# Kernel tuning notes

Hardware: AMD Instinct MI355X
Metric: run time of the kernel (lower is better)

The kernel has to match this reference:

```python
import jax, jax.numpy as jnp
import numpy as np

N_QUBITS = 12
LAYERS = 3


def _apply(state, mats, axes):
    """Apply batched k-qubit gate. state: [B]+[2]*n complex64; mats: [B, 2^k, 2^k]; axes: state axes (1-based)."""
    k = len(axes)
    d = 2 ** k
    s = jnp.moveaxis(state, axes, tuple(range(1, k + 1)))
    shp = s.shape
    s = jnp.einsum('bij,bjk->bik', mats, s.reshape(shp[0], d, -1))
    return jnp.moveaxis(s.reshape(shp), tuple(range(1, k + 1)), axes)


def _ry(theta):
    # RY(theta) = [[cos(t/2), -sin(t/2)], [sin(t/2), cos(t/2)]], batched over B
    c = jnp.cos(theta / 2).astype(jnp.complex64)
    s = jnp.sin(theta / 2).astype(jnp.complex64)
    return jnp.stack([jnp.stack([c, -s], -1), jnp.stack([s, c], -1)], -2)


def _crx(theta):
    # CRX: identity on control=0 subspace, RX(theta) on control=1 subspace (basis order |ct>)
    c = jnp.cos(theta / 2).astype(jnp.complex64)
    s = (-1j) * jnp.sin(theta / 2).astype(jnp.complex64)
    o = jnp.ones_like(c)
    z = jnp.zeros_like(c)
    rows = [[o, z, z, z], [z, o, z, z], [z, z, c, s], [z, z, s, c]]
    return jnp.stack([jnp.stack(r, -1) for r in rows], -2)


def _circuit(state_re, state_im, params):
    B = params.shape[0]
    n = N_QUBITS
    state = (state_re + 1j * state_im).astype(jnp.complex64).reshape((B,) + (2,) * n)
    p = params.reshape(B, LAYERS, 4, n)  # param idx order: RY block, CRX block, RY block, CRX block
    for l in range(LAYERS):
        th = p[:, l]
        for w in range(n):
            state = _apply(state, _ry(th[:, 0, w]), (w + 1,))
        for i, w in enumerate(reversed(range(n))):
            state = _apply(state, _crx(th[:, 1, i]), (w + 1, ((w + 1) % n) + 1))
        for w in range(n):
            state = _apply(state, _ry(th[:, 2, w]), (w + 1,))
        for i, w in enumerate([n - 1] + list(range(n - 1))):
            state = _apply(state, _crx(th[:, 3, i]), (w + 1, ((w - 1) % n) + 1))
    state = state.reshape(B, -1)
    return jnp.stack([state.real, state.imag], -1)  # [B, 2^n, 2]


def setup_inputs() -> dict:
    key = jax.random.key(0)
    k1, k2, k3 = jax.random.split(key, 3)
    B = 128
    dim = 2 ** N_QUBITS
    return {
        'state_re': jax.random.normal(k1, (B, dim), jnp.float32),
        'state_im': jax.random.normal(k2, (B, dim), jnp.float32),
        'params': jax.random.normal(k3, (B, LAYERS * 4 * N_QUBITS), jnp.float32),
    }


def reference(state_re, state_im, params):
    return _circuit(state_re, state_im, params)
```

## Files before the change

### kernel.cpp

```cpp
#include <hip/hip_runtime.h>
#include <math.h>

#define DIM  4096
#define BLK  512
#define NPAR 144

typedef float v2f __attribute__((ext_vector_type(2)));

struct Ph { int reg[3]; int wav[3]; };
struct TMap { unsigned pk[9]; unsigned short so[8]; unsigned short rn[8]; };

constexpr int REGS[12][3] = {
  {11,0,1},{1,2,3},{3,4,5},{5,6,7},{7,8,9},{9,10,11},
  {11,0,1},{9,10,11},{7,8,9},{5,6,7},{3,4,5},{1,2,3}};

constexpr Ph phaseAt(int i) {
  Ph p = {};
  if (i == 0 || i == 37) {
    p.reg[0]=0; p.reg[1]=1; p.reg[2]=2;
    p.wav[0]=9; p.wav[1]=10; p.wav[2]=11;
    return p;
  }
  int e = (i - 1) % 12;
  for (int j = 0; j < 3; ++j) p.reg[j] = REGS[e][j];
  bool A = (e <= 2) || (e >= 10);
  p.wav[0] = A ? 6 : 2; p.wav[1] = A ? 7 : 3; p.wav[2] = A ? 8 : 4;
  return p;
}
constexpr bool inArr(const int* a, int n, int b) {
  for (int i = 0; i < n; ++i) if (a[i] == b) return true;
  return false;
}
constexpr int idxOf3(const int* a, int v) {
  for (int j = 0; j < 3; ++j) if (a[j] == v) return j;
  return -1;
}
constexpr bool isLoc(int t) {
  if (t == 0 || t == 36) return false;
  Ph a = phaseAt(t), b = phaseAt(t + 1);
  return a.wav[0]==b.wav[0] && a.wav[1]==b.wav[1] && a.wav[2]==b.wav[2];
}
constexpr int bufIdx(int t) {
  int k = 0;
  for (int u = 0; u <= t; ++u) if (!isLoc(u)) ++k;
  return (k + 1) & 1;
}
constexpr int sharedBit(Ph o, Ph n) {
  for (int j = 0; j < 3; ++j) if (inArr(n.reg, 3, o.reg[j])) return o.reg[j];
  return -1;
}

struct BuildOut { TMap m; int js, jn; bool ok; };

constexpr BuildOut buildT(Ph o, Ph n, bool local) {
  BuildOut R = {};
  R.ok = true;
  int s = sharedBit(o, n);
  if (s < 0) { R.ok = false; return R; }
  R.js = idxOf3(o.reg, s);
  R.jn = idxOf3(n.reg, s);
  if (R.js < 0 || R.jn < 0) { R.ok = false; return R; }
  bool lo[12] = {}, ln[12] = {};
  for (int b = 0; b < 12; ++b) {
    lo[b] = !inArr(o.reg,3,b) && !inArr(o.wav,3,b);
    ln[b] = !inArr(n.reg,3,b) && !inArr(n.wav,3,b);
  }
  int col[12] = {};
  bool uo[12] = {}, un[12] = {}, consumed[12] = {};
  col[s] = 1; consumed[s] = true;
  int row = 1;
  for (int b = 0; b < 12 && row < 4; ++b)
    if (lo[b] && ln[b]) { col[b] = 1 << row; uo[b]=un[b]=true; consumed[b]=true; ++row; }
  while (row < 4) {
    int a = -1, c = -1;
    for (int b = 0; b < 12; ++b) if (lo[b] && !uo[b] && !consumed[b]) { a = b; break; }
    for (int b = 0; b < 12; ++b) if (ln[b] && !un[b] && !consumed[b] && b != a) { c = b; break; }
    if (a < 0 || c < 0) { R.ok = false; return R; }
    col[a] |= 1 << row; col[c] |= 1 << row;
    uo[a]=true; un[c]=true; consumed[c]=true;
    ++row;
  }
  if (local) {
    for (int i = 0; i < 3; ++i) {
      if (consumed[o.wav[i]]) { R.ok = false; return R; }
      col[o.wav[i]] |= 1 << (9 + i);
      consumed[o.wav[i]] = true;
    }
    int rr = 4;
    for (int b = 0; b < 12; ++b) if (!consumed[b]) { col[b] |= 1 << rr; ++rr; }
    if (rr != 9) { R.ok = false; return R; }
  } else {
    int rr = 4;
    for (int b = 0; b < 12; ++b) if (!consumed[b]) { col[b] |= 1 << rr; ++rr; }
    if (rr != 12) { R.ok = false; return R; }
  }
  {
    int pv[12] = {}, pb[12] = {};
    int nr = 0;
    for (int b = 0; b < 12; ++b) {
      int v = col[b];
      for (int k = 0; k < nr; ++k) if (v & pb[k]) v ^= pv[k];
      if (v) { pb[nr] = v & (-v); pv[nr] = v; ++nr; }
    }
    if (nr != 12) { R.ok = false; return R; }
  }
  int Lo[6] = {}, Ln[6] = {};
  int i0 = 0, i1 = 0;
  for (int b = 0; b < 12; ++b) { if (lo[b]) Lo[i0++] = b; if (ln[b]) Ln[i1++] = b; }
  if (i0 != 6 || i1 != 6) { R.ok = false; return R; }
  for (int i = 0; i < 9; ++i) {
    unsigned po = (i < 6) ? (unsigned)col[Lo[i]] : (unsigned)col[o.wav[i-6]];
    unsigned pn = (i < 6) ? (unsigned)col[Ln[i]] : (unsigned)col[n.wav[i-6]];
    R.m.pk[i] = po | (pn << 16);
  }
  for (int r = 0; r < 8; ++r) {
    int a = 0, c = 0;
    for (int j = 0; j < 3; ++j)
      if ((r >> j) & 1) { a ^= col[o.reg[j]]; c ^= col[n.reg[j]]; }
    R.m.so[r] = (unsigned short)(a * 8);
    R.m.rn[r] = (unsigned short)(c * 8);
  }
  return R;
}

struct AllT { TMap t[37]; bool loc[37]; int buf[37]; int js[37]; int jn[37]; bool ok; };
constexpr AllT buildAll() {
  AllT A = {};
  A.ok = true;
  for (int t = 0; t < 37; ++t) {
    BuildOut b = buildT(phaseAt(t), phaseAt(t + 1), isLoc(t));
    A.t[t] = b.m;
    A.ok = A.ok && b.ok;
    A.loc[t] = isLoc(t);
    A.buf[t] = bufIdx(t);
    A.js[t] = b.js;
    A.jn[t] = b.jn;
  }
  return A;
}
constexpr AllT AT = buildAll();
static_assert(AT.ok, "slot-map construction failed");

template<int J>
__device__ __forceinline__ void ry8(v2f (&z)[8], v2f a) {
  const float c = a.x, s = a.y;
  #pragma unroll
  for (int p = 0; p < 4; ++p) {
    const int r0 = ((p & ~((1 << J) - 1)) << 1) | (p & ((1 << J) - 1));
    const int r1 = r0 | (1 << J);
    v2f u = z[r0], v = z[r1];
    z[r0] = c * u - s * v;
    z[r1] = s * u + c * v;
  }
}
template<int JC, int JT>
__device__ __forceinline__ void crx8(v2f (&z)[8], v2f a) {
  const float c = a.x, s = a.y;
  constexpr int MC = 1 << JC, MT = 1 << JT;
  constexpr int mlo = MC < MT ? MC : MT;
  constexpr int mhi = MC < MT ? MT : MC;
  #pragma unroll
  for (int p = 0; p < 2; ++p) {
    int q = ((p & ~(mlo - 1)) << 1) | (p & (mlo - 1));
    q = ((q & ~(mhi - 1)) << 1) | (q & (mhi - 1));
    const int r0 = q | MC, r1 = r0 | MT;
    v2f u = z[r0], v = z[r1];
    v2f n0, n1;
    n0.x = c * u.x + s * v.y;
    n0.y = c * u.y - s * v.x;
    n1.x = c * v.x + s * u.y;
    n1.y = c * v.y - s * u.x;
    z[r0] = n0; z[r1] = n1;
  }
}

template<int E>
__device__ __forceinline__ void gates(v2f (&z)[8], const v2f* ang, int base) {
  auto A = [&](int k) { return ang[base + k]; };
  if constexpr (E == 0)      { ry8<0>(z,A(0));  ry8<1>(z,A(11)); ry8<2>(z,A(10));
                               crx8<1,0>(z,A(12)); crx8<2,1>(z,A(13)); }
  else if constexpr (E == 1) { ry8<1>(z,A(9));  ry8<2>(z,A(8));
                               crx8<1,0>(z,A(14)); crx8<2,1>(z,A(15)); }
  else if constexpr (E == 2) { ry8<1>(z,A(7));  ry8<2>(z,A(6));
                               crx8<1,0>(z,A(16)); crx8<2,1>(z,A(17)); }
  else if constexpr (E == 3) { ry8<1>(z,A(5));  ry8<2>(z,A(4));
                               crx8<1,0>(z,A(18)); crx8<2,1>(z,A(19)); }
  else if constexpr (E == 4) { ry8<1>(z,A(3));  ry8<2>(z,A(2));
                               crx8<1,0>(z,A(20)); crx8<2,1>(z,A(21)); }
  else if constexpr (E == 5) { ry8<1>(z,A(1));
                               crx8<1,0>(z,A(22)); crx8<2,1>(z,A(23)); }
  else if constexpr (E == 6) { ry8<0>(z,A(24)); ry8<1>(z,A(35)); ry8<2>(z,A(34));
                               crx8<1,2>(z,A(36)); crx8<0,1>(z,A(37)); }
  else if constexpr (E == 7) { ry8<0>(z,A(26)); ry8<1>(z,A(25));
                               crx8<1,2>(z,A(38)); crx8<0,1>(z,A(39)); }
  else if constexpr (E == 8) { ry8<0>(z,A(28)); ry8<1>(z,A(27));
                               crx8<1,2>(z,A(40)); crx8<0,1>(z,A(41)); }
  else if constexpr (E == 9) { ry8<0>(z,A(30)); ry8<1>(z,A(29));
                               crx8<1,2>(z,A(42)); crx8<0,1>(z,A(43)); }
  else if constexpr (E == 10){ ry8<0>(z,A(32)); ry8<1>(z,A(31));
                               crx8<1,2>(z,A(44)); crx8<0,1>(z,A(45)); }
  else                       { ry8<1>(z,A(33));
                               crx8<1,2>(z,A(46)); crx8<0,1>(z,A(47)); }
}

template<int T>
__device__ __forceinline__ void restage(v2f (&z)[8], int tid, char* Lb, char* C0, char* C1) {
  constexpr bool LOC = AT.loc[T];
  constexpr int JS = AT.js[T], JN = AT.jn[T];
  char* buf = LOC ? Lb : (AT.buf[T] ? C1 : C0);
  unsigned acc = 0;
  #pragma unroll
  for (int i = 0; i < 9; ++i)
    acc ^= (unsigned)(-((tid >> i) & 1)) & AT.t[T].pk[i];
  const unsigned bo = (acc & 0xfffu) << 3;
  const unsigned bn = ((acc >> 16) & 0xfffu) << 3;
  #pragma unroll
  for (int r = 0; r < 8; ++r) {
    if (r & (1 << JS)) continue;
    v2f z0 = z[r], z1 = z[r | (1 << JS)];
    float4 w; w.x = z0.x; w.y = z0.y; w.z = z1.x; w.w = z1.y;
    *(float4*)(buf + (bo ^ AT.t[T].so[r])) = w;
  }
  if (LOC) {
    asm volatile("" ::: "memory");
  } else {
    __syncthreads();
  }
  #pragma unroll
  for (int r = 0; r < 8; ++r) {
    if (r & (1 << JN)) continue;
    float4 w = *(const float4*)(buf + (bn ^ AT.t[T].rn[r]));
    v2f z0, z1;
    z0.x = w.x; z0.y = w.y;
    z1.x = w.z; z1.y = w.w;
    z[r] = z0;
    z[r | (1 << JN)] = z1;
  }
}

template<int L>
__device__ __forceinline__ void layer(v2f (&z)[8], int tid, const v2f* ang,
                                      char* Lb, char* C0, char* C1) {
  const int base = 48 * L;
  gates<0>(z, ang, base);  restage<12*L + 1>(z, tid, Lb, C0, C1);
  gates<1>(z, ang, base);  restage<12*L + 2>(z, tid, Lb, C0, C1);
  gates<2>(z, ang, base);  restage<12*L + 3>(z, tid, Lb, C0, C1);
  gates<3>(z, ang, base);  restage<12*L + 4>(z, tid, Lb, C0, C1);
  gates<4>(z, ang, base);  restage<12*L + 5>(z, tid, Lb, C0, C1);
  gates<5>(z, ang, base);  restage<12*L + 6>(z, tid, Lb, C0, C1);
  gates<6>(z, ang, base);  restage<12*L + 7>(z, tid, Lb, C0, C1);
  gates<7>(z, ang, base);  restage<12*L + 8>(z, tid, Lb, C0, C1);
  gates<8>(z, ang, base);  restage<12*L + 9>(z, tid, Lb, C0, C1);
  gates<9>(z, ang, base);  restage<12*L + 10>(z, tid, Lb, C0, C1);
  gates<10>(z, ang, base); restage<12*L + 11>(z, tid, Lb, C0, C1);
  gates<11>(z, ang, base);
  if constexpr (L < 2) restage<12*L + 12>(z, tid, Lb, C0, C1);
}

__global__ __launch_bounds__(BLK) void ansatz_kernel(
    const float* __restrict__ sre, const float* __restrict__ sim,
    const float* __restrict__ params, float* __restrict__ out) {

  __shared__ alignas(16) v2f C0s[DIM], C1s[DIM], Ls[DIM];
  __shared__ v2f ang[NPAR];

  const int b = blockIdx.x, tid = threadIdx.x;
  char* C0 = (char*)C0s;
  char* C1 = (char*)C1s;
  char* Lb = (char*)Ls;

  if (tid < NPAR) {
    float s, c;
    sincosf(0.5f * params[b * NPAR + tid], &s, &c);
    v2f a; a.x = c; a.y = s;
    ang[tid] = a;
  }

  v2f z[8];
  {
    const float4* pr = (const float4*)(sre + b * DIM + (tid << 3));
    const float4* pi = (const float4*)(sim + b * DIM + (tid << 3));
    float4 fr0 = pr[0], fr1 = pr[1];
    float4 fi0 = pi[0], fi1 = pi[1];
    z[0].x = fr0.x; z[0].y = fi0.x;
    z[1].x = fr0.y; z[1].y = fi0.y;
    z[2].x = fr0.z; z[2].y = fi0.z;
    z[3].x = fr0.w; z[3].y = fi0.w;
    z[4].x = fr1.x; z[4].y = fi1.x;
    z[5].x = fr1.y; z[5].y = fi1.y;
    z[6].x = fr1.z; z[6].y = fi1.z;
    z[7].x = fr1.w; z[7].y = fi1.w;
    restage<0>(z, tid, Lb, C0, C1);
  }

  layer<0>(z, tid, ang, Lb, C0, C1);
  layer<1>(z, tid, ang, Lb, C0, C1);
  layer<2>(z, tid, ang, Lb, C0, C1);

  restage<36>(z, tid, Lb, C0, C1);
  v2f* o2 = (v2f*)out + (size_t)b * DIM + (tid << 3);
  #pragma unroll
  for (int r = 0; r < 8; r += 2) {
    float4 w;
    w.x = z[r].x;     w.y = z[r].y;
    w.z = z[r + 1].x; w.w = z[r + 1].y;
    *(float4*)(o2 + r) = w;
  }
}

extern "C" void kernel_launch(void* const* d_in, const int* in_sizes, int n_in,
                              void* d_out, int out_size, void* d_ws, size_t ws_size,
                              hipStream_t stream) {
  const float* sre    = (const float*)d_in[0];
  const float* sim    = (const float*)d_in[1];
  const float* params = (const float*)d_in[2];
  float* out          = (float*)d_out;

  const int B = in_sizes[0] / DIM;
  ansatz_kernel<<<B, BLK, 0, stream>>>(sre, sim, params, out);
}
```

Before: 80.74 us.

## Load/store state directly in gate layout and broadcast angles via readlane

After: 78.91 us, median of 2. 1.02x faster.

```diff
diff --git a/kernel.cpp b/kernel.cpp
--- a/kernel.cpp
+++ b/kernel.cpp
@@ -70,7 +70,7 @@
   col[s] = 1; consumed[s] = true;
   int row = 1;
   for (int b = 0; b < 12 && row < 4; ++b)
-    if (lo[b] && ln[b]) { col[b] = 1 << row; uo[b]=un[b]=true; consumed[b]=true; ++row; }
+    if (lo[b] && ln[b] && !consumed[b]) { col[b] = 1 << row; uo[b]=un[b]=true; consumed[b]=true; ++row; }
   while (row < 4) {
     int a = -1, c = -1;
     for (int b = 0; b < 12; ++b) if (lo[b] && !uo[b] && !consumed[b]) { a = b; break; }
@@ -141,6 +141,17 @@
 constexpr AllT AT = buildAll();
 static_assert(AT.ok, "slot-map construction failed");
 
+__device__ __forceinline__ float rlf(float v, int l) {
+  return __int_as_float(__builtin_amdgcn_readlane(__float_as_int(v), l));
+}
+template<int AO>
+__device__ __forceinline__ v2f angAt(const float (&ct)[3], const float (&st)[3]) {
+  v2f a;
+  a.x = rlf(ct[AO >> 6], AO & 63);
+  a.y = rlf(st[AO >> 6], AO & 63);
+  return a;
+}
+
 template<int J>
 __device__ __forceinline__ void ry8(v2f (&z)[8], v2f a) {
   const float c = a.x, s = a.y;
@@ -174,9 +185,9 @@
   }
 }
 
-template<int E>
-__device__ __forceinline__ void gates(v2f (&z)[8], const v2f* ang, int base) {
-  auto A = [&](int k) { return ang[base + k]; };
+template<int E, int L>
+__device__ __forceinline__ void gates(v2f (&z)[8], const float (&ct)[3], const float (&st)[3]) {
+#define A(k) (angAt<48 * L + (k)>(ct, st))
   if constexpr (E == 0)      { ry8<0>(z,A(0));  ry8<1>(z,A(11)); ry8<2>(z,A(10));
                                crx8<1,0>(z,A(12)); crx8<2,1>(z,A(13)); }
   else if constexpr (E == 1) { ry8<1>(z,A(9));  ry8<2>(z,A(8));
@@ -201,6 +212,7 @@
                                crx8<1,2>(z,A(44)); crx8<0,1>(z,A(45)); }
   else                       { ry8<1>(z,A(33));
                                crx8<1,2>(z,A(46)); crx8<0,1>(z,A(47)); }
+#undef A
 }
 
 template<int T>
@@ -239,21 +251,21 @@
 }
 
 template<int L>
-__device__ __forceinline__ void layer(v2f (&z)[8], int tid, const v2f* ang,
+__device__ __forceinline__ void layer(v2f (&z)[8], int tid,
+                                      const float (&ct)[3], const float (&st)[3],
                                       char* Lb, char* C0, char* C1) {
-  const int base = 48 * L;
-  gates<0>(z, ang, base);  restage<12*L + 1>(z, tid, Lb, C0, C1);
-  gates<1>(z, ang, base);  restage<12*L + 2>(z, tid, Lb, C0, C1);
-  gates<2>(z, ang, base);  restage<12*L + 3>(z, tid, Lb, C0, C1);
-  gates<3>(z, ang, base);  restage<12*L + 4>(z, tid, Lb, C0, C1);
-  gates<4>(z, ang, base);  restage<12*L + 5>(z, tid, Lb, C0, C1);
-  gates<5>(z, ang, base);  restage<12*L + 6>(z, tid, Lb, C0, C1);
-  gates<6>(z, ang, base);  restage<12*L + 7>(z, tid, Lb, C0, C1);
-  gates<7>(z, ang, base);  restage<12*L + 8>(z, tid, Lb, C0, C1);
-  gates<8>(z, ang, base);  restage<12*L + 9>(z, tid, Lb, C0, C1);
-  gates<9>(z, ang, base);  restage<12*L + 10>(z, tid, Lb, C0, C1);
-  gates<10>(z, ang, base); restage<12*L + 11>(z, tid, Lb, C0, C1);
-  gates<11>(z, ang, base);
+  gates<0, L>(z, ct, st);  restage<12*L + 1>(z, tid, Lb, C0, C1);
+  gates<1, L>(z, ct, st);  restage<12*L + 2>(z, tid, Lb, C0, C1);
+  gates<2, L>(z, ct, st);  restage<12*L + 3>(z, tid, Lb, C0, C1);
+  gates<3, L>(z, ct, st);  restage<12*L + 4>(z, tid, Lb, C0, C1);
+  gates<4, L>(z, ct, st);  restage<12*L + 5>(z, tid, Lb, C0, C1);
+  gates<5, L>(z, ct, st);  restage<12*L + 6>(z, tid, Lb, C0, C1);
+  gates<6, L>(z, ct, st);  restage<12*L + 7>(z, tid, Lb, C0, C1);
+  gates<7, L>(z, ct, st);  restage<12*L + 8>(z, tid, Lb, C0, C1);
+  gates<8, L>(z, ct, st);  restage<12*L + 9>(z, tid, Lb, C0, C1);
+  gates<9, L>(z, ct, st);  restage<12*L + 10>(z, tid, Lb, C0, C1);
+  gates<10, L>(z, ct, st); restage<12*L + 11>(z, tid, Lb, C0, C1);
+  gates<11, L>(z, ct, st);
   if constexpr (L < 2) restage<12*L + 12>(z, tid, Lb, C0, C1);
 }
 
@@ -262,49 +274,50 @@
     const float* __restrict__ params, float* __restrict__ out) {
 
   __shared__ alignas(16) v2f C0s[DIM], C1s[DIM], Ls[DIM];
-  __shared__ v2f ang[NPAR];
 
   const int b = blockIdx.x, tid = threadIdx.x;
   char* C0 = (char*)C0s;
   char* C1 = (char*)C1s;
   char* Lb = (char*)Ls;
 
-  if (tid < NPAR) {
-    float s, c;
-    sincosf(0.5f * params[b * NPAR + tid], &s, &c);
-    v2f a; a.x = c; a.y = s;
-    ang[tid] = a;
+  float ct[3], st[3];
+  {
+    const int lane = tid & 63;
+    #pragma unroll
+    for (int j = 0; j < 3; ++j) {
+      int idx = lane + 64 * j;
+      int ci = (idx < NPAR) ? idx : 0;
+      float th = params[(size_t)b * NPAR + ci];
+      sincosf(0.5f * th, &st[j], &ct[j]);
+    }
   }
 
   v2f z[8];
   {
-    const float4* pr = (const float4*)(sre + b * DIM + (tid << 3));
-    const float4* pi = (const float4*)(sim + b * DIM + (tid << 3));
-    float4 fr0 = pr[0], fr1 = pr[1];
-    float4 fi0 = pi[0], fi1 = pi[1];
-    z[0].x = fr0.x; z[0].y = fi0.x;
-    z[1].x = fr0.y; z[1].y = fi0.y;
-    z[2].x = fr0.z; z[2].y = fi0.z;
-    z[3].x = fr0.w; z[3].y = fi0.w;
-    z[4].x = fr1.x; z[4].y = fi1.x;
-    z[5].x = fr1.y; z[5].y = fi1.y;
-    z[6].x = fr1.z; z[6].y = fi1.z;
-    z[7].x = fr1.w; z[7].y = fi1.w;
-    restage<0>(z, tid, Lb, C0, C1);
-  }
-
-  layer<0>(z, tid, ang, Lb, C0, C1);
-  layer<1>(z, tid, ang, Lb, C0, C1);
-  layer<2>(z, tid, ang, Lb, C0, C1);
-
-  restage<36>(z, tid, Lb, C0, C1);
-  v2f* o2 = (v2f*)out + (size_t)b * DIM + (tid << 3);
-  #pragma unroll
-  for (int r = 0; r < 8; r += 2) {
-    float4 w;
-    w.x = z[r].x;     w.y = z[r].y;
-    w.z = z[r + 1].x; w.w = z[r + 1].y;
-    *(float4*)(o2 + r) = w;
+    int base = ((tid & 15) << 2) | ((tid & 16) << 5) | ((tid & 32) << 5)
+             | (tid & 64) | (tid & 128) | (tid & 256);
+    const float4* pr = (const float4*)(sre + (size_t)b * DIM + base);
+    const float4* pi = (const float4*)(sim + (size_t)b * DIM + base);
+    float4 f0 = pr[0], f1 = pr[512];
+    float4 g0 = pi[0], g1 = pi[512];
+    z[0].x = f0.x; z[0].y = g0.x;  z[2].x = f0.y; z[2].y = g0.y;
+    z[4].x = f0.z; z[4].y = g0.z;  z[6].x = f0.w; z[6].y = g0.w;
+    z[1].x = f1.x; z[1].y = g1.x;  z[3].x = f1.y; z[3].y = g1.y;
+    z[5].x = f1.z; z[5].y = g1.z;  z[7].x = f1.w; z[7].y = g1.w;
+  }
+
+  layer<0>(z, tid, ct, st, Lb, C0, C1);
+  layer<1>(z, tid, ct, st, Lb, C0, C1);
+  layer<2>(z, tid, ct, st, Lb, C0, C1);
+
+  {
+    int base = (tid & 1) | ((tid & 2) << 3) | ((tid & 4) << 3)
+             | ((tid & 8) << 6) | ((tid & 16) << 6) | ((tid & 32) << 6)
+             | (tid & 64) | (tid & 128) | (tid & 256);
+    v2f* o2 = (v2f*)out + (size_t)b * DIM + base;
+    #pragma unroll
+    for (int r = 0; r < 8; ++r)
+      o2[2 * r] = z[r];
   }
 }
 
```
